# Performance work log

Measured on AMD Instinct MI355X. Metric: run time of the kernel, lower is better.

## Reference

```python
import jax, jax.numpy as jnp
import numpy as np

HEADS = 16
DIM_HEAD = 64


def setup_inputs() -> dict:
    key = jax.random.key(0)
    k1, k2, k3, k4, k5 = jax.random.split(key, 5)
    B, S, E = 4, 2048, 1024
    inner = HEADS * DIM_HEAD  # 1024
    return {
        "hidden_states": jax.random.normal(k1, (B, S, E), dtype=jnp.float32),
        "w_q": jax.random.normal(k2, (E, inner), dtype=jnp.float32) * (E ** -0.5),
        "w_k": jax.random.normal(k3, (E, inner), dtype=jnp.float32) * (E ** -0.5),
        "w_v": jax.random.normal(k4, (E, inner), dtype=jnp.float32) * (E ** -0.5),
        "w_o": jax.random.normal(k5, (inner, E), dtype=jnp.float32) * (inner ** -0.5),
    }


def reference(hidden_states, w_q, w_k, w_v, w_o):
    # Self-attention path: context = hidden_states (context arg is None).
    B, S, _ = hidden_states.shape
    dtype = hidden_states.dtype
    scale = DIM_HEAD ** -0.5

    q = (hidden_states @ w_q).reshape(B, S, HEADS, DIM_HEAD)
    k = (hidden_states @ w_k).reshape(B, S, HEADS, DIM_HEAD)
    v = (hidden_states @ w_v).reshape(B, S, HEADS, DIM_HEAD)

    # fp32 softmax as in the original module
    q32 = q.astype(jnp.float32)
    k32 = k.astype(jnp.float32)
    scores = jnp.einsum('btnh,bfnh->bnft', k32, q32) * scale  # [B, H, S_q, S_kv]
    probs = jax.nn.softmax(scores, axis=-1).astype(dtype)

    out = jnp.einsum('bnft,btnh->bfnh', probs, v)  # [B, S, H, D]
    out = out.reshape(B, S, HEADS * DIM_HEAD)
    return out @ w_o  # [B, S, query_dim]
```

## Files before the change

### kernel.cpp

```cpp
#include <hip/hip_runtime.h>
#include <stdint.h>

typedef __attribute__((ext_vector_type(8))) unsigned short ushort8;
typedef __attribute__((ext_vector_type(8))) __bf16 bf16x8;
typedef __attribute__((ext_vector_type(4))) float f32x4;
typedef __attribute__((ext_vector_type(4))) uint32_t u32x4;

__device__ __forceinline__ unsigned short f2bf(float f) {
  union { float f; uint32_t u; } x; x.f = f;
  uint32_t u = x.u;
  uint32_t r = (u + 0x7fffu + ((u >> 16) & 1u)) >> 16;
  return (unsigned short)r;
}

__device__ __forceinline__ uint32_t pack_bf2(float lo, float hi) {
  return (uint32_t)f2bf(lo) | ((uint32_t)f2bf(hi) << 16);
}

__device__ __forceinline__ uint32_t rhu2(float lo, float hi) {
  union { float f; uint32_t u; } a, b; a.f = lo; b.f = hi;
  return __builtin_amdgcn_perm(b.u + 0x8000u, a.u + 0x8000u, 0x07060302u);
}

__device__ __forceinline__ void store_c(unsigned short* p, float v) { *p = f2bf(v); }
__device__ __forceinline__ void store_c(float* p, float v) { *p = v; }

__device__ __forceinline__ void gll16(const unsigned short* g, unsigned short* l) {
  __builtin_amdgcn_global_load_lds((const __attribute__((address_space(1))) void*)g,
                                   (__attribute__((address_space(3))) void*)l,
                                   16, 0, 0);
}

__global__ __launch_bounds__(256) void cvt_f32_bf16(
    const float* __restrict__ x, unsigned short* __restrict__ y, int n4) {
  int i = blockIdx.x * 256 + threadIdx.x;
  if (i >= n4) return;
  float4 v = *(const float4*)(x + (size_t)i * 4);
  uint2 p; p.x = pack_bf2(v.x, v.y); p.y = pack_bf2(v.z, v.w);
  *(uint2*)(y + (size_t)i * 4) = p;
}

__device__ __forceinline__ void transpose_body(const float* W, unsigned short* WT) {
  __shared__ unsigned short tile[32][33];
  int c0 = blockIdx.x * 32, r0 = blockIdx.y * 32;
  int x = threadIdx.x, y = threadIdx.y;
#pragma unroll
  for (int i = 0; i < 32; i += 8)
    tile[y + i][x] = f2bf(W[(size_t)(r0 + y + i) * 1024 + c0 + x]);
  __syncthreads();
#pragma unroll
  for (int i = 0; i < 32; i += 8)
    WT[(size_t)(c0 + y + i) * 1024 + r0 + x] = tile[x][y + i];
}

__global__ void transpose_w(const float* __restrict__ W,
                            unsigned short* __restrict__ WT) {
  transpose_body(W, WT);
}

__global__ void transpose_w3(const float* W0, const float* W1, const float* W2,
                             unsigned short* T0, unsigned short* T1,
                             unsigned short* T2) {
  const float* W = (blockIdx.z == 0) ? W0 : (blockIdx.z == 1) ? W1 : W2;
  unsigned short* WT = (blockIdx.z == 0) ? T0 : (blockIdx.z == 1) ? T1 : T2;
  transpose_body(W, WT);
}

template <typename OutT>
__global__ __launch_bounds__(256, 2) void gemm3(
    const unsigned short* A,
    const unsigned short* BT0, const unsigned short* BT1, const unsigned short* BT2,
    OutT* C0, OutT* C1, OutT* C2,
    int M, int N, int K, float sc0) {
  const unsigned short* BT = (blockIdx.z == 0) ? BT0 : (blockIdx.z == 1) ? BT1 : BT2;
  OutT* C = (blockIdx.z == 0) ? C0 : (blockIdx.z == 1) ? C1 : C2;
  const float sc = (blockIdx.z == 0) ? sc0 : 1.0f;

  __shared__ __attribute__((aligned(16))) unsigned short As[2][128 * 64];
  __shared__ __attribute__((aligned(16))) unsigned short Bs[2][128 * 64];

  const int tid = threadIdx.x;
  const int wave = tid >> 6, lane = tid & 63;
  const int fr = lane & 15, fq = lane >> 4;
  const int wm = wave >> 1, wn = wave & 1;
  const int bm = blockIdx.x * 128, bn = blockIdx.y * 128;

  const int r8 = tid >> 3, c8 = tid & 7;
  const int s8 = c8 ^ (r8 & 7);
  const unsigned short* Ag = A + (size_t)(bm + r8) * K + s8 * 8;
  const unsigned short* Bg = BT + (size_t)(bn + r8) * K + s8 * 8;

  f32x4 acc[4][4] = {};
  const int rx = fr & 7;

  const int NT = K >> 6;

#pragma unroll
  for (int i = 0; i < 4; i++) {
    gll16(Ag + (size_t)(i * 32) * K, &As[0][(i * 32 + wave * 8) * 64]);
    gll16(Bg + (size_t)(i * 32) * K, &Bs[0][(i * 32 + wave * 8) * 64]);
  }

  int cur = 0;
  for (int t = 0; t < NT; ++t) {
    __syncthreads();

    if (t + 1 < NT) {
      const int b = cur ^ 1;
      const size_t k0 = (size_t)(t + 1) * 64;
#pragma unroll
      for (int i = 0; i < 4; i++) {
        gll16(Ag + k0 + (size_t)(i * 32) * K, &As[b][(i * 32 + wave * 8) * 64]);
        gll16(Bg + k0 + (size_t)(i * 32) * K, &Bs[b][(i * 32 + wave * 8) * 64]);
      }
    }

#pragma unroll
    for (int kh = 0; kh < 2; ++kh) {
      bf16x8 af[4], bfr[4];
#pragma unroll
      for (int mt = 0; mt < 4; mt++)
        af[mt] = *(const bf16x8*)&As[cur][(wm * 64 + mt * 16 + fr) * 64 +
                                          (((kh * 4 + fq) ^ rx) * 8)];
#pragma unroll
      for (int nt = 0; nt < 4; nt++)
        bfr[nt] = *(const bf16x8*)&Bs[cur][(wn * 64 + nt * 16 + fr) * 64 +
                                           (((kh * 4 + fq) ^ rx) * 8)];
#pragma unroll
      for (int mt = 0; mt < 4; mt++)
#pragma unroll
        for (int nt = 0; nt < 4; nt++)
          acc[mt][nt] = __builtin_amdgcn_mfma_f32_16x16x32_bf16(af[mt], bfr[nt], acc[mt][nt], 0, 0, 0);
    }
    cur ^= 1;
  }

#pragma unroll
  for (int mt = 0; mt < 4; mt++)
#pragma unroll
    for (int nt = 0; nt < 4; nt++)
#pragma unroll
      for (int r = 0; r < 4; r++) {
        int row = bm + wm * 64 + mt * 16 + fq * 4 + r;
        int col = bn + wn * 64 + nt * 16 + fr;
        store_c(&C[(size_t)row * N + col], acc[mt][nt][r] * sc);
      }
}

__global__ __launch_bounds__(256, 4) void attn_kernel(
    const unsigned short* q, const unsigned short* k,
    const unsigned short* v, unsigned short* o) {
  const int S = 2048, E = 1024;
  __shared__ __attribute__((aligned(16))) unsigned short Ksb[2 * 64 * 64];
  __shared__ __attribute__((aligned(16))) unsigned short Vtb[64 * 64];

  const int tid = threadIdx.x;
  const int wave = tid >> 6, lane = tid & 63;
  const int fr = lane & 15, fq = lane >> 4;
  const int q0 = blockIdx.x * 128;
  const int bh = blockIdx.y;
  const int b = bh >> 4, h = bh & 15;
  const size_t base = ((size_t)b * S) * E + (size_t)h * 64;

  bf16x8 aq[2][2];
#pragma unroll
  for (int qg = 0; qg < 2; qg++)
#pragma unroll
    for (int ks = 0; ks < 2; ks++)
      aq[qg][ks] = *(const bf16x8*)&q[base +
          (size_t)(q0 + qg * 64 + wave * 16 + fr) * E + ks * 32 + fq * 8];

  ushort8 ones_u;
#pragma unroll
  for (int j = 0; j < 8; j++) ones_u[j] = 0x3F80;
  bf16x8 onesf = *(bf16x8*)&ones_u;

  f32x4 ot[2][4] = {};
  f32x4 osum[2] = {};

  const int srow = lane >> 3;
  const int scol = (((lane & 7) ^ srow) << 3);
  const unsigned short* Kg = k + base + (size_t)(wave * 16 + srow) * E + scol;

  const int rp = (tid & 31) * 2;
  const int dcv = (tid >> 5) * 8;
  const int u_ = rp & 31;
  const int slot = 32 * (rp >> 5) + 8 * ((u_ & 15) >> 2) + 4 * (u_ >> 4) + (u_ & 3);
  const unsigned short* Vg = v + base + (size_t)rp * E + dcv;

  const int rx = (fr & 7) << 3;

  gll16(Kg, &Ksb[wave * 1024]);
  gll16(Kg + 8 * (size_t)E, &Ksb[wave * 1024 + 512]);

  int cur = 0;
  for (int t = 0; t < 32; t++) {
    const int nxt = cur ^ 4096;

    const size_t toff = (size_t)t * 64 * E;
    u32x4 va = *(const u32x4*)(Vg + toff);
    u32x4 vb = *(const u32x4*)(Vg + toff + E);

    __syncthreads();

#pragma unroll
    for (int w = 0; w < 4; w++) {
      uint32_t lo = __builtin_amdgcn_perm(vb[w], va[w], 0x05040100u);
      uint32_t hi = __builtin_amdgcn_perm(vb[w], va[w], 0x07060302u);
      int d = dcv + 2 * w;
      *(uint32_t*)&Vtb[d * 64 + (slot ^ ((2 * w) << 3))] = lo;
      *(uint32_t*)&Vtb[(d + 1) * 64 + (slot ^ ((2 * w + 1) << 3))] = hi;
    }

    __syncthreads();

    if (t < 31) {
      const size_t poff = (size_t)(t + 1) * 64 * E;
      gll16(Kg + poff, &Ksb[nxt + wave * 1024]);
      gll16(Kg + poff + 8 * (size_t)E, &Ksb[nxt + wave * 1024 + 512]);
    }

    f32x4 st[2][4] = {};
    __builtin_amdgcn_s_setprio(1);
#pragma unroll
    for (int ks = 0; ks < 2; ks++) {
#pragma unroll
      for (int tt = 0; tt < 4; tt++) {
        bf16x8 ak = *(const bf16x8*)&Ksb[cur + (tt * 16 + fr) * 64 +
                                         ((ks * 32 + fq * 8) ^ rx)];
        st[0][tt] = __builtin_amdgcn_mfma_f32_16x16x32_bf16(ak, aq[0][ks], st[0][tt], 0, 0, 0);
        st[1][tt] = __builtin_amdgcn_mfma_f32_16x16x32_bf16(ak, aq[1][ks], st[1][tt], 0, 0, 0);
      }
    }
    __builtin_amdgcn_s_setprio(0);

    uint32_t pk[2][4][2];
#pragma unroll
    for (int qg = 0; qg < 2; qg++)
#pragma unroll
      for (int tt = 0; tt < 4; tt++) {
        float e0 = __builtin_amdgcn_exp2f(st[qg][tt][0]);
        float e1 = __builtin_amdgcn_exp2f(st[qg][tt][1]);
        float e2 = __builtin_amdgcn_exp2f(st[qg][tt][2]);
        float e3 = __builtin_amdgcn_exp2f(st[qg][tt][3]);
        pk[qg][tt][0] = rhu2(e0, e1);
        pk[qg][tt][1] = rhu2(e2, e3);
      }

    __builtin_amdgcn_s_setprio(1);
#pragma unroll
    for (int c = 0; c < 2; c++) {
      bf16x8 bp[2];
#pragma unroll
      for (int qg = 0; qg < 2; qg++) {
        u32x4 bpr;
        bpr[0] = pk[qg][2 * c][0];
        bpr[1] = pk[qg][2 * c][1];
        bpr[2] = pk[qg][2 * c + 1][0];
        bpr[3] = pk[qg][2 * c + 1][1];
        bp[qg] = *(bf16x8*)&bpr;
      }
#pragma unroll
      for (int dt = 0; dt < 4; dt++) {
        bf16x8 av = *(const bf16x8*)&Vtb[(dt * 16 + fr) * 64 +
                                         ((c * 32 + fq * 8) ^ rx)];
        ot[0][dt] = __builtin_amdgcn_mfma_f32_16x16x32_bf16(av, bp[0], ot[0][dt], 0, 0, 0);
        ot[1][dt] = __builtin_amdgcn_mfma_f32_16x16x32_bf16(av, bp[1], ot[1][dt], 0, 0, 0);
      }
      osum[0] = __builtin_amdgcn_mfma_f32_16x16x32_bf16(onesf, bp[0], osum[0], 0, 0, 0);
      osum[1] = __builtin_amdgcn_mfma_f32_16x16x32_bf16(onesf, bp[1], osum[1], 0, 0, 0);
    }
    __builtin_amdgcn_s_setprio(0);

    cur = nxt;
  }

#pragma unroll
  for (int qg = 0; qg < 2; qg++) {
    float inv = 1.0f / osum[qg][0];
    size_t rowbase = base + (size_t)(q0 + qg * 64 + wave * 16 + fr) * E;
#pragma unroll
    for (int dt = 0; dt < 4; dt++) {
      uint32_t w0 = rhu2(ot[qg][dt][0] * inv, ot[qg][dt][1] * inv);
      uint32_t w1 = rhu2(ot[qg][dt][2] * inv, ot[qg][dt][3] * inv);
      *(uint32_t*)&o[rowbase + dt * 16 + fq * 4] = w0;
      *(uint32_t*)&o[rowbase + dt * 16 + fq * 4 + 2] = w1;
    }
  }
}

extern "C" void kernel_launch(void* const* d_in, const int* in_sizes, int n_in,
                              void* d_out, int out_size, void* d_ws, size_t ws_size,
                              hipStream_t stream) {
  const float* hs = (const float*)d_in[0];
  const float* wq = (const float*)d_in[1];
  const float* wk = (const float*)d_in[2];
  const float* wv = (const float*)d_in[3];
  const float* wo = (const float*)d_in[4];
  unsigned short* ws = (unsigned short*)d_ws;

  unsigned short* wqT = ws;
  unsigned short* wkT = ws + 1048576;
  unsigned short* wvT = ws + 2097152;
  unsigned short* woT = wqT;
  unsigned short* qb  = ws + 3145728;
  unsigned short* kb  = qb + 8388608;
  unsigned short* vb  = kb + 8388608;
  unsigned short* ob  = qb;
  unsigned short* hsb = (unsigned short*)d_out;
  float* out = (float*)d_out;

  const int M = 8192, N = 1024, K = 1024;
  const float KSC = 0.125f * 1.44269504088896341f;

  cvt_f32_bf16<<<dim3(M * K / 4 / 256), 256, 0, stream>>>(hs, hsb, M * K / 4);

  dim3 tb(32, 8);
  transpose_w3<<<dim3(32, 32, 3), tb, 0, stream>>>(wq, wk, wv, wqT, wkT, wvT);

  gemm3<unsigned short><<<dim3(M / 128, N / 128, 3), 256, 0, stream>>>(
      hsb, wqT, wkT, wvT, qb, kb, vb, M, N, K, KSC);

  transpose_w<<<dim3(32, 32), tb, 0, stream>>>(wo, woT);

  attn_kernel<<<dim3(2048 / 128, 64), 256, 0, stream>>>(qb, kb, vb, ob);

  gemm3<float><<<dim3(M / 128, N / 128, 1), 256, 0, stream>>>(
      ob, woT, woT, woT, out, out, out, M, N, K, 1.0f);
}
```

Before: 264.4 us.

## Restructure GEMM into triple-buffered BK=32 pipeline with XCD-aware block remapping

Replaces the double-buffered BK=64 GEMM with a three-stage pipeline over BK=32 tiles. It uses explicit vmcnt waits and raw barriers so two tile loads stay in flight while the current one is computed. It also remaps block indices so consecutive blocks on the same XCD share A rows across the Q/K/V outputs, improving L2 reuse. LDS per block shrinks, so occupancy rises to three blocks per CU, at the cost of more barriers per K-step and hand-written waitcnt logic that must match the number of outstanding loads.

```diff
diff --git a/kernel.cpp b/kernel.cpp
--- a/kernel.cpp
+++ b/kernel.cpp
@@ -67,72 +67,80 @@
 }
 
 template <typename OutT>
-__global__ __launch_bounds__(256, 2) void gemm3(
+__global__ __launch_bounds__(256, 3) void gemm4(
     const unsigned short* A,
     const unsigned short* BT0, const unsigned short* BT1, const unsigned short* BT2,
     OutT* C0, OutT* C1, OutT* C2,
-    int M, int N, int K, float sc0) {
-  const unsigned short* BT = (blockIdx.z == 0) ? BT0 : (blockIdx.z == 1) ? BT1 : BT2;
-  OutT* C = (blockIdx.z == 0) ? C0 : (blockIdx.z == 1) ? C1 : C2;
-  const float sc = (blockIdx.z == 0) ? sc0 : 1.0f;
-
-  __shared__ __attribute__((aligned(16))) unsigned short As[2][128 * 64];
-  __shared__ __attribute__((aligned(16))) unsigned short Bs[2][128 * 64];
+    int M, int N, int K, float sc0, int nby) {
+  const int total = gridDim.x * gridDim.y;
+  const int orig = blockIdx.y * gridDim.x + blockIdx.x;
+  const int per8 = total >> 3;
+  const int my = (orig & 7) * per8 + (orig >> 3);
+  const int nsub = gridDim.x;
+  const int bxi = my / nsub;
+  const int sub = my - bxi * nsub;
+  const int z = sub / nby;
+  const int byi = sub - z * nby;
+
+  const unsigned short* BT = (z == 0) ? BT0 : (z == 1) ? BT1 : BT2;
+  OutT* C = (z == 0) ? C0 : (z == 1) ? C1 : C2;
+  const float sc = (z == 0) ? sc0 : 1.0f;
+
+  __shared__ __attribute__((aligned(16))) unsigned short As[3][128 * 32];
+  __shared__ __attribute__((aligned(16))) unsigned short Bs[3][128 * 32];
 
   const int tid = threadIdx.x;
   const int wave = tid >> 6, lane = tid & 63;
   const int fr = lane & 15, fq = lane >> 4;
   const int wm = wave >> 1, wn = wave & 1;
-  const int bm = blockIdx.x * 128, bn = blockIdx.y * 128;
-
-  const int r8 = tid >> 3, c8 = tid & 7;
-  const int s8 = c8 ^ (r8 & 7);
-  const unsigned short* Ag = A + (size_t)(bm + r8) * K + s8 * 8;
-  const unsigned short* Bg = BT + (size_t)(bn + r8) * K + s8 * 8;
+  const int bm = bxi * 128, bn = byi * 128;
+
+  const int r4 = lane >> 2, c4 = lane & 3;
+  const int scs = (c4 ^ (r4 & 3)) * 8;
+  const unsigned short* Ag = A + (size_t)(bm + wave * 16 + r4) * K + scs;
+  const unsigned short* Bg = BT + (size_t)(bn + wave * 16 + r4) * K + scs;
 
   f32x4 acc[4][4] = {};
-  const int rx = fr & 7;
-
-  const int NT = K >> 6;
-
-#pragma unroll
-  for (int i = 0; i < 4; i++) {
-    gll16(Ag + (size_t)(i * 32) * K, &As[0][(i * 32 + wave * 8) * 64]);
-    gll16(Bg + (size_t)(i * 32) * K, &Bs[0][(i * 32 + wave * 8) * 64]);
-  }
-
-  int cur = 0;
+  const int NT = K >> 5;
+
+  auto STAGE = [&](int buf, int t) {
+    const size_t k0 = (size_t)t * 32;
+    gll16(Ag + k0, &As[buf][(wave * 16) * 32]);
+    gll16(Ag + k0 + (size_t)64 * K, &As[buf][(64 + wave * 16) * 32]);
+    gll16(Bg + k0, &Bs[buf][(wave * 16) * 32]);
+    gll16(Bg + k0 + (size_t)64 * K, &Bs[buf][(64 + wave * 16) * 32]);
+  };
+
+  const int rxr = (fq ^ (fr & 3)) * 8;
+
+  STAGE(0, 0);
+  STAGE(1, 1);
+
+  int bc = 0, bs = 2;
   for (int t = 0; t < NT; ++t) {
-    __syncthreads();
-
-    if (t + 1 < NT) {
-      const int b = cur ^ 1;
-      const size_t k0 = (size_t)(t + 1) * 64;
-#pragma unroll
-      for (int i = 0; i < 4; i++) {
-        gll16(Ag + k0 + (size_t)(i * 32) * K, &As[b][(i * 32 + wave * 8) * 64]);
-        gll16(Bg + k0 + (size_t)(i * 32) * K, &Bs[b][(i * 32 + wave * 8) * 64]);
-      }
-    }
-
-#pragma unroll
-    for (int kh = 0; kh < 2; ++kh) {
-      bf16x8 af[4], bfr[4];
-#pragma unroll
-      for (int mt = 0; mt < 4; mt++)
-        af[mt] = *(const bf16x8*)&As[cur][(wm * 64 + mt * 16 + fr) * 64 +
-                                          (((kh * 4 + fq) ^ rx) * 8)];
+    if (t + 1 < NT)
+      asm volatile("s_waitcnt vmcnt(4)" ::: "memory");
+    else
+      asm volatile("s_waitcnt vmcnt(0)" ::: "memory");
+    __builtin_amdgcn_s_barrier();
+
+    if (t + 2 < NT) STAGE(bs, t + 2);
+
+    bf16x8 af[4], bfr[4];
+#pragma unroll
+    for (int mt = 0; mt < 4; mt++)
+      af[mt] = *(const bf16x8*)&As[bc][(wm * 64 + mt * 16 + fr) * 32 + rxr];
+#pragma unroll
+    for (int nt = 0; nt < 4; nt++)
+      bfr[nt] = *(const bf16x8*)&Bs[bc][(wn * 64 + nt * 16 + fr) * 32 + rxr];
+#pragma unroll
+    for (int mt = 0; mt < 4; mt++)
 #pragma unroll
       for (int nt = 0; nt < 4; nt++)
-        bfr[nt] = *(const bf16x8*)&Bs[cur][(wn * 64 + nt * 16 + fr) * 64 +
-                                           (((kh * 4 + fq) ^ rx) * 8)];
-#pragma unroll
-      for (int mt = 0; mt < 4; mt++)
-#pragma unroll
-        for (int nt = 0; nt < 4; nt++)
-          acc[mt][nt] = __builtin_amdgcn_mfma_f32_16x16x32_bf16(af[mt], bfr[nt], acc[mt][nt], 0, 0, 0);
-    }
-    cur ^= 1;
+        acc[mt][nt] = __builtin_amdgcn_mfma_f32_16x16x32_bf16(af[mt], bfr[nt], acc[mt][nt], 0, 0, 0);
+
+    bc = (bc == 2) ? 0 : bc + 1;
+    bs = (bs == 2) ? 0 : bs + 1;
   }
 
 #pragma unroll
@@ -318,13 +326,13 @@
   dim3 tb(32, 8);
   transpose_w3<<<dim3(32, 32, 3), tb, 0, stream>>>(wq, wk, wv, wqT, wkT, wvT);
 
-  gemm3<unsigned short><<<dim3(M / 128, N / 128, 3), 256, 0, stream>>>(
-      hsb, wqT, wkT, wvT, qb, kb, vb, M, N, K, KSC);
+  gemm4<unsigned short><<<dim3(24, 64), 256, 0, stream>>>(
+      hsb, wqT, wkT, wvT, qb, kb, vb, M, N, K, KSC, 8);
 
   transpose_w<<<dim3(32, 32), tb, 0, stream>>>(wo, woT);
 
   attn_kernel<<<dim3(2048 / 128, 64), 256, 0, stream>>>(qb, kb, vb, ob);
 
-  gemm3<float><<<dim3(M / 128, N / 128, 1), 256, 0, stream>>>(
-      ob, woT, woT, woT, out, out, out, M, N, K, 1.0f);
-}
+  gemm4<float><<<dim3(8, 64), 256, 0, stream>>>(
+      ob, woT, woT, woT, out, out, out, M, N, K, 1.0f, 8);
+}
```

New measurement: 273.0 us. +3.2%, slower.

## Rework GEMM into 256x128 tiles with triple-buffered interleaved async prefetch

Applied to the files above, without the earlier changes.

Moves the projection GEMMs to 512-thread blocks computing 256x128 output tiles, staging through a 3-slot LDS ring with a two-tile prefetch distance. Global-to-LDS loads are split into parts and interleaved with the MFMA k-halves, using explicit vmcnt waits and raw barriers in place of __syncthreads. MFMA sections run at raised wave priority. The aim is to hide load latency and reduce per-block B-tile reloads, at the cost of more LDS per block (144KB across both buffers) and lower occupancy.

```diff
diff --git a/kernel.cpp b/kernel.cpp
--- a/kernel.cpp
+++ b/kernel.cpp
@@ -67,72 +67,91 @@
 }
 
 template <typename OutT>
-__global__ __launch_bounds__(256, 2) void gemm3(
+__global__ __launch_bounds__(512, 2) void gemm5(
     const unsigned short* A,
     const unsigned short* BT0, const unsigned short* BT1, const unsigned short* BT2,
     OutT* C0, OutT* C1, OutT* C2,
     int M, int N, int K, float sc0) {
-  const unsigned short* BT = (blockIdx.z == 0) ? BT0 : (blockIdx.z == 1) ? BT1 : BT2;
-  OutT* C = (blockIdx.z == 0) ? C0 : (blockIdx.z == 1) ? C1 : C2;
-  const float sc = (blockIdx.z == 0) ? sc0 : 1.0f;
-
-  __shared__ __attribute__((aligned(16))) unsigned short As[2][128 * 64];
-  __shared__ __attribute__((aligned(16))) unsigned short Bs[2][128 * 64];
+  const int z = blockIdx.z;
+  const unsigned short* BT = (z == 0) ? BT0 : (z == 1) ? BT1 : BT2;
+  OutT* C = (z == 0) ? C0 : (z == 1) ? C1 : C2;
+  const float sc = (z == 0) ? sc0 : 1.0f;
+
+  __shared__ __attribute__((aligned(16))) unsigned short As[3 * 256 * 64];
+  __shared__ __attribute__((aligned(16))) unsigned short Bs[3 * 128 * 64];
 
   const int tid = threadIdx.x;
   const int wave = tid >> 6, lane = tid & 63;
   const int fr = lane & 15, fq = lane >> 4;
   const int wm = wave >> 1, wn = wave & 1;
-  const int bm = blockIdx.x * 128, bn = blockIdx.y * 128;
+  const int bm = blockIdx.y * 256, bn = blockIdx.x * 128;
 
   const int r8 = tid >> 3, c8 = tid & 7;
-  const int s8 = c8 ^ (r8 & 7);
-  const unsigned short* Ag = A + (size_t)(bm + r8) * K + s8 * 8;
-  const unsigned short* Bg = BT + (size_t)(bn + r8) * K + s8 * 8;
+  const int s8 = (c8 ^ (r8 & 7)) * 8;
+  const unsigned short* Ag = A + (size_t)(bm + r8) * K + s8;
+  const unsigned short* Bg = BT + (size_t)(bn + r8) * K + s8;
+
+  const int NT = K >> 6;
+
+  auto stage = [&](int tile, int part) {
+    if (tile >= NT) return;
+    const int slot = tile % 3;
+    const size_t k0 = (size_t)tile * 64;
+    if (part < 4) {
+      gll16(Ag + k0 + (size_t)(part * 64) * K,
+            &As[slot * (256 * 64) + (part * 64 + 8 * wave) * 64]);
+    } else {
+      const int p = part - 4;
+      gll16(Bg + k0 + (size_t)(p * 64) * K,
+            &Bs[slot * (128 * 64) + (p * 64 + 8 * wave) * 64]);
+    }
+  };
 
   f32x4 acc[4][4] = {};
-  const int rx = fr & 7;
-
-  const int NT = K >> 6;
-
-#pragma unroll
-  for (int i = 0; i < 4; i++) {
-    gll16(Ag + (size_t)(i * 32) * K, &As[0][(i * 32 + wave * 8) * 64]);
-    gll16(Bg + (size_t)(i * 32) * K, &Bs[0][(i * 32 + wave * 8) * 64]);
-  }
-
-  int cur = 0;
+
+  stage(0, 0); stage(0, 1); stage(0, 2); stage(0, 3); stage(0, 4); stage(0, 5);
+  stage(1, 0); stage(1, 1); stage(1, 2); stage(1, 3);
+
   for (int t = 0; t < NT; ++t) {
-    __syncthreads();
-
-    if (t + 1 < NT) {
-      const int b = cur ^ 1;
-      const size_t k0 = (size_t)(t + 1) * 64;
-#pragma unroll
-      for (int i = 0; i < 4; i++) {
-        gll16(Ag + k0 + (size_t)(i * 32) * K, &As[b][(i * 32 + wave * 8) * 64]);
-        gll16(Bg + k0 + (size_t)(i * 32) * K, &Bs[b][(i * 32 + wave * 8) * 64]);
-      }
-    }
+    if (t + 1 < NT)
+      asm volatile("s_waitcnt vmcnt(4)" ::: "memory");
+    else
+      asm volatile("s_waitcnt vmcnt(0)" ::: "memory");
+    __builtin_amdgcn_s_barrier();
+    __builtin_amdgcn_sched_barrier(0);
+
+    const unsigned short* Asl = &As[(t % 3) * (256 * 64)];
+    const unsigned short* Bsl = &Bs[(t % 3) * (128 * 64)];
 
 #pragma unroll
     for (int kh = 0; kh < 2; ++kh) {
+      if (kh == 0) {
+        stage(t + 1, 4); stage(t + 1, 5); stage(t + 2, 0);
+      } else {
+        stage(t + 2, 1); stage(t + 2, 2); stage(t + 2, 3);
+      }
+
       bf16x8 af[4], bfr[4];
 #pragma unroll
       for (int mt = 0; mt < 4; mt++)
-        af[mt] = *(const bf16x8*)&As[cur][(wm * 64 + mt * 16 + fr) * 64 +
-                                          (((kh * 4 + fq) ^ rx) * 8)];
+        af[mt] = *(const bf16x8*)&Asl[(wm * 64 + mt * 16 + fr) * 64 +
+                                      (((kh * 4 + fq) ^ (fr & 7)) * 8)];
 #pragma unroll
       for (int nt = 0; nt < 4; nt++)
-        bfr[nt] = *(const bf16x8*)&Bs[cur][(wn * 64 + nt * 16 + fr) * 64 +
-                                           (((kh * 4 + fq) ^ rx) * 8)];
+        bfr[nt] = *(const bf16x8*)&Bsl[(wn * 64 + nt * 16 + fr) * 64 +
+                                       (((kh * 4 + fq) ^ (fr & 7)) * 8)];
+
+      __builtin_amdgcn_s_setprio(1);
 #pragma unroll
       for (int mt = 0; mt < 4; mt++)
 #pragma unroll
         for (int nt = 0; nt < 4; nt++)
-          acc[mt][nt] = __builtin_amdgcn_mfma_f32_16x16x32_bf16(af[mt], bfr[nt], acc[mt][nt], 0, 0, 0);
-    }
-    cur ^= 1;
+          acc[mt][nt] = __builtin_amdgcn_mfma_f32_16x16x32_bf16(
+              af[mt], bfr[nt], acc[mt][nt], 0, 0, 0);
+      __builtin_amdgcn_s_setprio(0);
+
+      if (kh == 0) __builtin_amdgcn_s_barrier();
+    }
   }
 
 #pragma unroll
@@ -318,13 +337,13 @@
   dim3 tb(32, 8);
   transpose_w3<<<dim3(32, 32, 3), tb, 0, stream>>>(wq, wk, wv, wqT, wkT, wvT);
 
-  gemm3<unsigned short><<<dim3(M / 128, N / 128, 3), 256, 0, stream>>>(
+  gemm5<unsigned short><<<dim3(8, 32, 3), 512, 0, stream>>>(
       hsb, wqT, wkT, wvT, qb, kb, vb, M, N, K, KSC);
 
   transpose_w<<<dim3(32, 32), tb, 0, stream>>>(wo, woT);
 
   attn_kernel<<<dim3(2048 / 128, 64), 256, 0, stream>>>(qb, kb, vb, ob);
 
-  gemm3<float><<<dim3(M / 128, N / 128, 1), 256, 0, stream>>>(
+  gemm5<float><<<dim3(8, 32, 1), 512, 0, stream>>>(
       ob, woT, woT, woT, out, out, out, M, N, K, 1.0f);
 }
```

New measurement: 311.1 us. 17.6% more time.
